# Kernel optimization log

Hardware: AMD Instinct MI355X
Metric: run time of the kernel (lower is better)

## Reference

```python
import jax, jax.numpy as jnp
import numpy as np
import math

C, NH, HD, L, P, FFN = 256, 8, 32, 1, 4, 512
H_BEV, W_BEV = 200, 100
NQ, BS, NV = 1000, 4, H_BEV * W_BEV
EPS = 1e-5


def _ln(x, g, b):
    m = x.mean(-1, keepdims=True)
    v = ((x - m) ** 2).mean(-1, keepdims=True)
    return (x - m) / jnp.sqrt(v + EPS) * g + b


def _mha(x, qpos, in_w, in_b, ow, ob):
    # nn.MultiheadAttention self-attention; key_pos = query_pos (shapes match)
    q = x + qpos
    k = x + qpos
    v = x
    wq, wk, wv = jnp.split(in_w, 3, axis=0)
    bq, bk, bv = jnp.split(in_b, 3, axis=0)
    bs, nq, _ = x.shape
    qh = (q @ wq.T + bq).reshape(bs, nq, NH, HD)
    kh = (k @ wk.T + bk).reshape(bs, nq, NH, HD)
    vh = (v @ wv.T + bv).reshape(bs, nq, NH, HD)
    scores = jnp.einsum('bqhd,bkhd->bhqk', qh, kh) / jnp.sqrt(jnp.float32(HD))
    attn = jax.nn.softmax(scores, axis=-1)
    out = jnp.einsum('bhqk,bkhd->bqhd', attn, vh).reshape(bs, nq, C)
    return out @ ow.T + ob


def _msdeform(x, qpos, value, ref, spatial_shapes, so_w, so_b, aw_w, aw_b, vp_w, vp_b, op_w, op_b):
    # Multi-scale deformable attention (single level), bilinear sampling with
    # align_corners=False convention and zero padding, as in the CUDA kernel.
    bs, nq, _ = x.shape
    q = x + qpos
    v = (value @ vp_w.T + vp_b).reshape(bs, NV, NH, HD).transpose(0, 2, 1, 3)  # [bs,nh,nv,hd]
    off = (q @ so_w.T + so_b).reshape(bs, nq, NH, L, P, 2)
    aw = jax.nn.softmax((q @ aw_w.T + aw_b).reshape(bs, nq, NH, L * P), axis=-1)
    aw = aw.reshape(bs, nq, NH, L, P)
    norm = jnp.stack([spatial_shapes[:, 1], spatial_shapes[:, 0]], -1).astype(jnp.float32)  # [L,2] = (W,H)
    loc = ref[:, :, None, :, None, :] + off / norm[None, None, None, :, None, :]  # [bs,nq,nh,L,P,2]
    loc = loc[:, :, :, 0]  # single level -> [bs,nq,nh,P,2]
    awp = aw[:, :, :, 0]   # [bs,nq,nh,P]
    x_im = loc[..., 0] * W_BEV - 0.5
    y_im = loc[..., 1] * H_BEV - 0.5
    x0 = jnp.floor(x_im)
    y0 = jnp.floor(y_im)
    lx = x_im - x0
    ly = y_im - y0
    x0i = x0.astype(jnp.int32)
    y0i = y0.astype(jnp.int32)
    acc = jnp.zeros((bs, NH, nq, P, HD), jnp.float32)
    for dy in (0, 1):
        for dx in (0, 1):
            xi = x0i + dx
            yi = y0i + dy
            w = (lx if dx else 1.0 - lx) * (ly if dy else 1.0 - ly)  # [bs,nq,nh,P]
            ok = ((xi >= 0) & (xi < W_BEV) & (yi >= 0) & (yi < H_BEV)).astype(jnp.float32)
            idx = jnp.clip(yi, 0, H_BEV - 1) * W_BEV + jnp.clip(xi, 0, W_BEV - 1)
            idx_t = idx.transpose(0, 2, 1, 3).reshape(bs, NH, nq * P)
            g = jnp.take_along_axis(v, idx_t[..., None], axis=2).reshape(bs, NH, nq, P, HD)
            acc = acc + g * (w * ok).transpose(0, 2, 1, 3)[..., None]
    out = (acc * awp.transpose(0, 2, 1, 3)[..., None]).sum(3)  # [bs,nh,nq,hd]
    out = out.transpose(0, 2, 1, 3).reshape(bs, nq, C)
    return out @ op_w.T + op_b


def setup_inputs() -> dict:
    key = jax.random.key(0)
    ks = jax.random.split(key, 24)
    f32 = jnp.float32

    def w(k, shp):
        fan = shp[-1]
        return (jax.random.normal(k, shp, f32) * (1.0 / np.sqrt(fan))).astype(f32)

    # sampling_offsets bias per _reset_parameters (radial grid init)
    thetas = np.arange(NH, dtype=np.float32) * (2.0 * math.pi / NH)
    grid = np.stack([np.cos(thetas), np.sin(thetas)], -1)
    grid = grid / np.abs(grid).max(-1, keepdims=True)
    grid = np.tile(grid[:, None, None, :], (1, L, P, 1))
    for i in range(P):
        grid[:, :, i, :] *= i + 1
    so_b = jnp.asarray(grid.reshape(-1), f32)

    return {
        'query': jax.random.normal(ks[0], (NQ, BS, C), f32),
        'value': jax.random.normal(ks[1], (NV, BS, C), f32),
        'query_pos': jax.random.normal(ks[2], (NQ, BS, C), f32),
        'reference_points': jax.random.uniform(ks[3], (BS, NQ, L, 2), f32),
        'spatial_shapes': jnp.array([[H_BEV, W_BEV]], jnp.int32),
        'level_start_index': jnp.zeros((L,), jnp.int32),
        'in_proj_w': w(ks[4], (3 * C, C)),
        'in_proj_b': jnp.zeros((3 * C,), f32),
        'mha_ow': w(ks[5], (C, C)),
        'mha_ob': jnp.zeros((C,), f32),
        'so_w': w(ks[6], (NH * L * P * 2, C)) * 0.01,
        'so_b': so_b,
        'aw_w': w(ks[7], (NH * L * P, C)) * 0.01,
        'aw_b': jnp.zeros((NH * L * P,), f32),
        'vp_w': w(ks[8], (C, C)),
        'vp_b': jnp.zeros((C,), f32),
        'op_w': w(ks[9], (C, C)),
        'op_b': jnp.zeros((C,), f32),
        'ffn_w1': w(ks[10], (FFN, C)),
        'ffn_b1': jnp.zeros((FFN,), f32),
        'ffn_w2': w(ks[11], (C, FFN)),
        'ffn_b2': jnp.zeros((C,), f32),
        'ln1_g': jnp.ones((C,), f32), 'ln1_b': jnp.zeros((C,), f32),
        'ln2_g': jnp.ones((C,), f32), 'ln2_b': jnp.zeros((C,), f32),
        'ln3_g': jnp.ones((C,), f32), 'ln3_b': jnp.zeros((C,), f32),
    }


def reference(query, value, query_pos, reference_points, spatial_shapes, level_start_index,
              in_proj_w, in_proj_b, mha_ow, mha_ob, so_w, so_b, aw_w, aw_b,
              vp_w, vp_b, op_w, op_b, ffn_w1, ffn_b1, ffn_w2, ffn_b2,
              ln1_g, ln1_b, ln2_g, ln2_b, ln3_g, ln3_b):
    # batch_first=False: (seq, bs, C) -> (bs, seq, C)
    x = query.transpose(1, 0, 2)
    val = value.transpose(1, 0, 2)
    qpos = query_pos.transpose(1, 0, 2)
    # self_attn -> norm (residual inside attn wrapper; dropout=0 in eval)
    x = _ln(x + _mha(x, qpos, in_proj_w, in_proj_b, mha_ow, mha_ob), ln1_g, ln1_b)
    # cross_attn (MSDeformAttn) -> norm
    x = _ln(x + _msdeform(x, qpos, val, reference_points, spatial_shapes,
                          so_w, so_b, aw_w, aw_b, vp_w, vp_b, op_w, op_b), ln2_g, ln2_b)
    # ffn -> norm
    h = jax.nn.relu(x @ ffn_w1.T + ffn_b1) @ ffn_w2.T + ffn_b2
    x = _ln(x + h, ln3_g, ln3_b)
    return x.transpose(1, 0, 2)
```

## Files before the change

### kernel.cpp

```cpp
#include <hip/hip_runtime.h>
#include <hip/hip_bf16.h>
#include <cmath>

#define BS   4
#define NQ   1000
#define CDIM 256
#define NH   8
#define HD   32
#define NVAL 20000
#define FFND 512
#define PN   4
#define WBEV 100
#define HBEV 200
#define TK   32

typedef __bf16 v8bf __attribute__((ext_vector_type(8)));
typedef float  v4f  __attribute__((ext_vector_type(4)));

__device__ __forceinline__ void gload_lds16(const void* g, void* l) {
    __builtin_amdgcn_global_load_lds(
        (const __attribute__((address_space(1))) unsigned int*)g,
        (__attribute__((address_space(3))) unsigned int*)l, 16, 0, 0);
}

__device__ __forceinline__ void vgemm_block(
    int vb, const float* __restrict__ value, const __bf16* __restrict__ Wv,
    const float* __restrict__ bv, __bf16* __restrict__ vpj, char* smem)
{
    __bf16* As = (__bf16*)smem;
    __bf16* Bs = (__bf16*)(smem + 16384);
    int tid = threadIdx.x;
    int wave = tid >> 6, lane = tid & 63, quad = lane >> 4, n16 = lane & 15;
    int bm = (vb >> 1) * 128, bn = (vb & 1) * 128;
    int wm = (wave & 1) * 64, wn = (wave >> 1) * 64;
    v4f acc[4][4] = {};

    for (int k0 = 0; k0 < 256; k0 += 64) {
        float4 fa[4][2];
        #pragma unroll
        for (int i = 0; i < 4; i++) {
            int e = i * 256 + tid;
            int r = e >> 3, c = (e & 7) ^ (r & 7);
            const float* p = value + (long)(bm + r) * 256 + k0 + c * 8;
            fa[i][0] = *(const float4*)p;
            fa[i][1] = *(const float4*)(p + 4);
        }
        __syncthreads();
        #pragma unroll
        for (int i = 0; i < 4; i++) {
            int e = i * 256 + tid;
            v8bf v;
            v[0] = (__bf16)fa[i][0].x; v[1] = (__bf16)fa[i][0].y;
            v[2] = (__bf16)fa[i][0].z; v[3] = (__bf16)fa[i][0].w;
            v[4] = (__bf16)fa[i][1].x; v[5] = (__bf16)fa[i][1].y;
            v[6] = (__bf16)fa[i][1].z; v[7] = (__bf16)fa[i][1].w;
            *(v8bf*)(As + e * 8) = v;
        }
        #pragma unroll
        for (int i = 0; i < 4; i++) {
            int e = i * 256 + tid;
            int r = e >> 3, c = (e & 7) ^ (r & 7);
            gload_lds16(Wv + (long)(bn + r) * 256 + k0 + c * 8, Bs + e * 8);
        }
        __syncthreads();
        #pragma unroll
        for (int s = 0; s < 2; s++) {
            v8bf af[4], bfr[4];
            #pragma unroll
            for (int mi = 0; mi < 4; mi++) {
                int row = wm + mi * 16 + n16;
                af[mi] = *(v8bf*)&As[row * 64 + (((quad + s * 4) ^ (row & 7))) * 8];
            }
            #pragma unroll
            for (int nj = 0; nj < 4; nj++) {
                int row = wn + nj * 16 + n16;
                bfr[nj] = *(v8bf*)&Bs[row * 64 + (((quad + s * 4) ^ (row & 7))) * 8];
            }
            #pragma unroll
            for (int mi = 0; mi < 4; mi++)
                #pragma unroll
                for (int nj = 0; nj < 4; nj++)
                    acc[mi][nj] = __builtin_amdgcn_mfma_f32_16x16x32_bf16(af[mi], bfr[nj], acc[mi][nj], 0, 0, 0);
        }
    }
    #pragma unroll
    for (int mi = 0; mi < 4; mi++) {
        #pragma unroll
        for (int r = 0; r < 4; r++) {
            int m = bm + wm + mi * 16 + quad * 4 + r;
            #pragma unroll
            for (int nj = 0; nj < 4; nj++) {
                int nn = bn + wn + nj * 16 + n16;
                vpj[(long)m * 256 + nn] = (__bf16)(acc[mi][nj][r] + bv[nn]);
            }
        }
    }
}

__global__ __launch_bounds__(256) void prep_all_kernel(
    const float* __restrict__ query, const float* __restrict__ qpos,
    const float* __restrict__ in_w, const float* __restrict__ mha_ow,
    const float* __restrict__ vp_w, const float* __restrict__ op_w,
    const float* __restrict__ ffn_w1, const float* __restrict__ ffn_w2,
    const float* __restrict__ so_w, const float* __restrict__ aw_w,
    const float* __restrict__ so_b, const float* __restrict__ aw_b,
    float* __restrict__ x, float* __restrict__ qpos_t,
    __bf16* __restrict__ x_bf, __bf16* __restrict__ xq_bf,
    __bf16* __restrict__ wb, __bf16* __restrict__ wsmall,
    float* __restrict__ bsmall)
{
    int blk = blockIdx.x, tid = threadIdx.x;
    if (blk < 640) {
        long e = ((long)blk * 256 + tid) * 4;
        const float* src; long off;
        if      (e < 196608) { src = in_w;   off = e; }
        else if (e < 262144) { src = mha_ow; off = e - 196608; }
        else if (e < 327680) { src = vp_w;   off = e - 262144; }
        else if (e < 393216) { src = op_w;   off = e - 327680; }
        else if (e < 524288) { src = ffn_w1; off = e - 393216; }
        else                 { src = ffn_w2; off = e - 524288; }
        float4 v = *(const float4*)(src + off);
        __bf16* d = wb + e;
        d[0] = (__bf16)v.x; d[1] = (__bf16)v.y; d[2] = (__bf16)v.z; d[3] = (__bf16)v.w;
    } else if (blk < 4640) {
        int qb = blk - 640;
        int q = qb / BS, b = qb % BS;
        float qv = query[(q * BS + b) * CDIM + tid];
        float pv = qpos [(q * BS + b) * CDIM + tid];
        int o = (b * NQ + q) * CDIM + tid;
        x[o] = qv; qpos_t[o] = pv;
        x_bf[o] = (__bf16)qv; xq_bf[o] = (__bf16)(qv + pv);
    } else if (blk < 4672) {
        long e = ((long)(blk - 4640) * 256 + tid) * 4;
        int row = (int)(e >> 8), col = (int)(e & 255);
        float4 v = {0.f, 0.f, 0.f, 0.f};
        if (row < 64)      v = *(const float4*)(so_w + row * 256 + col);
        else if (row < 96) v = *(const float4*)(aw_w + (row - 64) * 256 + col);
        __bf16* d = wsmall + e;
        d[0] = (__bf16)v.x; d[1] = (__bf16)v.y; d[2] = (__bf16)v.z; d[3] = (__bf16)v.w;
    } else {
        if (tid < 128) bsmall[tid] = tid < 64 ? so_b[tid] : (tid < 96 ? aw_b[tid - 64] : 0.f);
    }
}

template<int TBM, int TBN, bool RIDE>
__global__ __launch_bounds__(256) void mgemm_kernel(
    const __bf16* __restrict__ A, const __bf16* __restrict__ W,
    const float* __restrict__ bias, float* __restrict__ Yf,
    __bf16* __restrict__ Yb, int M, int N, int K, int relu, int nx, int nprim,
    const float* __restrict__ value, const __bf16* __restrict__ Wv,
    const float* __restrict__ bv, __bf16* __restrict__ vpj, int voff)
{
    constexpr int PRIM = TBM * 64 * 2 + TBN * 64 * 2;
    constexpr int SZ = RIDE ? (PRIM > 32768 ? PRIM : 32768) : PRIM;
    __shared__ __align__(16) char smem[SZ];
    if (RIDE && (int)blockIdx.x >= nprim) {
        vgemm_block(blockIdx.x - nprim + voff, value, Wv, bv, vpj, smem);
        return;
    }
    constexpr int WMF = TBM / 32;
    constexpr int WNF = TBN / 32;
    __bf16* As = (__bf16*)smem;
    __bf16* Bs = (__bf16*)(smem + TBM * 128);
    int bm = (blockIdx.x / nx) * TBM, bn = (blockIdx.x % nx) * TBN;
    int tid = threadIdx.x;
    int wave = tid >> 6, lane = tid & 63, quad = lane >> 4, n16 = lane & 15;
    int wm = (wave & 1) * (TBM / 2), wn = (wave >> 1) * (TBN / 2);
    v4f acc[WMF][WNF] = {};

    for (int k0 = 0; k0 < K; k0 += 64) {
        __syncthreads();
        #pragma unroll
        for (int i = 0; i < TBM * 8 / 256; i++) {
            int e = i * 256 + tid;
            int r = e >> 3, c = (e & 7) ^ (r & 7);
            int row = bm + r; if (row > M - 1) row = M - 1;
            gload_lds16(A + (long)row * K + k0 + c * 8, As + e * 8);
        }
        #pragma unroll
        for (int i = 0; i < TBN * 8 / 256; i++) {
            int e = i * 256 + tid;
            int r = e >> 3, c = (e & 7) ^ (r & 7);
            gload_lds16(W + (long)(bn + r) * K + k0 + c * 8, Bs + e * 8);
        }
        __syncthreads();
        #pragma unroll
        for (int s = 0; s < 2; s++) {
            v8bf af[WMF], bfr[WNF];
            #pragma unroll
            for (int mi = 0; mi < WMF; mi++) {
                int row = wm + mi * 16 + n16;
                af[mi] = *(v8bf*)&As[row * 64 + (((quad + s * 4) ^ (row & 7))) * 8];
            }
            #pragma unroll
            for (int nj = 0; nj < WNF; nj++) {
                int row = wn + nj * 16 + n16;
                bfr[nj] = *(v8bf*)&Bs[row * 64 + (((quad + s * 4) ^ (row & 7))) * 8];
            }
            #pragma unroll
            for (int mi = 0; mi < WMF; mi++)
                #pragma unroll
                for (int nj = 0; nj < WNF; nj++)
                    acc[mi][nj] = __builtin_amdgcn_mfma_f32_16x16x32_bf16(af[mi], bfr[nj], acc[mi][nj], 0, 0, 0);
        }
    }

    #pragma unroll
    for (int mi = 0; mi < WMF; mi++) {
        #pragma unroll
        for (int r = 0; r < 4; r++) {
            int m = bm + wm + mi * 16 + quad * 4 + r;
            if (m >= M) continue;
            #pragma unroll
            for (int nj = 0; nj < WNF; nj++) {
                int nn = bn + wn + nj * 16 + n16;
                if (nn >= N) continue;
                float v = acc[mi][nj][r] + bias[nn];
                if (relu) v = fmaxf(v, 0.f);
                if (Yf) Yf[(long)m * N + nn] = v;
                if (Yb) Yb[(long)m * N + nn] = (__bf16)v;
            }
        }
    }
}

__global__ __launch_bounds__(256) void qkvv_kernel(
    const __bf16* __restrict__ xq, const __bf16* __restrict__ xv,
    const __bf16* __restrict__ W, const float* __restrict__ bias,
    __bf16* __restrict__ qk, __bf16* __restrict__ vh,
    const float* __restrict__ value, const __bf16* __restrict__ Wv,
    const float* __restrict__ bv, __bf16* __restrict__ vpj, int voff)
{
    __shared__ __align__(16) char smem[32768];
    int tid = threadIdx.x;
    if (blockIdx.x >= 756) {
        vgemm_block(blockIdx.x - 756 + voff, value, Wv, bv, vpj, smem);
        return;
    }
    int blk = blockIdx.x;
    int bn = (blk % 12) * 64, bm = (blk / 12) * 64;
    __bf16* As = (__bf16*)smem;
    __bf16* Bs = (__bf16*)(smem + 8192);
    const __bf16* A = (bn < 512) ? xq : xv;
    int wave = tid >> 6, lane = tid & 63, quad = lane >> 4, n16 = lane & 15;
    int wm = (wave & 1) * 32, wn = (wave >> 1) * 32;
    v4f acc[2][2] = {};

    for (int k0 = 0; k0 < 256; k0 += 64) {
        __syncthreads();
        #pragma unroll
        for (int i = 0; i < 2; i++) {
            int e = i * 256 + tid;
            int r = e >> 3, c = (e & 7) ^ (r & 7);
            int row = bm + r; if (row > BS * NQ - 1) row = BS * NQ - 1;
            gload_lds16(A + (long)row * 256 + k0 + c * 8, As + e * 8);
        }
        #pragma unroll
        for (int i = 0; i < 2; i++) {
            int e = i * 256 + tid;
            int r = e >> 3, c = (e & 7) ^ (r & 7);
            gload_lds16(W + (long)(bn + r) * 256 + k0 + c * 8, Bs + e * 8);
        }
        __syncthreads();
        #pragma unroll
        for (int s = 0; s < 2; s++) {
            v8bf af[2], bfr[2];
            #pragma unroll
            for (int mi = 0; mi < 2; mi++) {
                int row = wm + mi * 16 + n16;
                af[mi] = *(v8bf*)&As[row * 64 + (((quad + s * 4) ^ (row & 7))) * 8];
            }
            #pragma unroll
            for (int nj = 0; nj < 2; nj++) {
                int row = wn + nj * 16 + n16;
                bfr[nj] = *(v8bf*)&Bs[row * 64 + (((quad + s * 4) ^ (row & 7))) * 8];
            }
            #pragma unroll
            for (int mi = 0; mi < 2; mi++)
                #pragma unroll
                for (int nj = 0; nj < 2; nj++)
                    acc[mi][nj] = __builtin_amdgcn_mfma_f32_16x16x32_bf16(af[mi], bfr[nj], acc[mi][nj], 0, 0, 0);
        }
    }

    #pragma unroll
    for (int mi = 0; mi < 2; mi++) {
        #pragma unroll
        for (int r = 0; r < 4; r++) {
            int m = bm + wm + mi * 16 + quad * 4 + r;
            if (m >= BS * NQ) continue;
            #pragma unroll
            for (int nj = 0; nj < 2; nj++) {
                int nn = bn + wn + nj * 16 + n16;
                float v = acc[mi][nj][r] + bias[nn];
                if (nn < 512) qk[(long)m * 512 + nn] = (__bf16)v;
                else          vh[(long)m * 256 + (nn - 512)] = (__bf16)v;
            }
        }
    }
}

__global__ __launch_bounds__(256) void fattnv_kernel(
    const __bf16* __restrict__ qk, const __bf16* __restrict__ vh,
    __bf16* __restrict__ aout,
    const float* __restrict__ value, const __bf16* __restrict__ Wv,
    const float* __restrict__ bv, __bf16* __restrict__ vpj, int voff)
{
    __shared__ __align__(16) char smem[32768];
    int tid = threadIdx.x;
    if (blockIdx.x >= 512) {
        vgemm_block(blockIdx.x - 512 + voff, value, Wv, bv, vpj, smem);
        return;
    }
    int fb = blockIdx.x;
    int qt = fb & 15, h = (fb >> 4) & 7, b = fb >> 7;
    __bf16* Ks = (__bf16*)smem;
    __bf16* Vt = (__bf16*)(smem + 5120);
    __bf16* Pl = (__bf16*)(smem + 10240);
    int wave = tid >> 6, lane = tid & 63, quad = lane >> 4, n = lane & 15;
    int q0 = qt * 64 + wave * 16;
    const float scale = 0.17677669529663687f;
    const float M0 = 8.0f;

    int qrow = q0 + n; if (qrow > NQ - 1) qrow = NQ - 1;
    v8bf aq = *(const v8bf*)(qk + (long)(b * NQ + qrow) * 512 + h * HD + quad * 8);

    v4f o0 = {}, o1 = {};
    float lp[4] = {0.f, 0.f, 0.f, 0.f};

    int sv = tid >> 7;
    int t2 = tid & 127;
    int key = t2 >> 2;
    int d8 = (t2 & 3) * 8;
    int vcol = key ^ (((d8 >> 3) & 1) << 4);

    auto loadtile = [&](int k0) -> v8bf {
        int krow = k0 + key; if (krow > NQ - 1) krow = NQ - 1;
        const __bf16* p = sv ? (vh + (long)(b * NQ + krow) * CDIM + h * HD + d8)
                             : (qk + (long)(b * NQ + krow) * 512 + 256 + h * HD + d8);
        return *(const v8bf*)p;
    };

    v8bf stg = loadtile(0);
    int pb = 0;
    for (int k0 = 0; k0 < NQ; k0 += TK) {
        if (sv == 0) {
            *(v8bf*)&Ks[(pb * TK + key) * 40 + d8] = stg;
        } else {
            #pragma unroll
            for (int j = 0; j < 8; j++) Vt[(pb * HD + d8 + j) * 40 + vcol] = stg[j];
        }
        if (k0 + TK < NQ) stg = loadtile(k0 + TK);
        __syncthreads();

        v8bf bk0 = *(v8bf*)&Ks[(pb * TK + n) * 40 + quad * 8];
        v8bf bk1 = *(v8bf*)&Ks[(pb * TK + 16 + n) * 40 + quad * 8];
        v4f z = {};
        v4f S0 = __builtin_amdgcn_mfma_f32_16x16x32_bf16(aq, bk0, z, 0, 0, 0);
        v4f S1 = __builtin_amdgcn_mfma_f32_16x16x32_bf16(aq, bk1, z, 0, 0, 0);

        bool last = (k0 + TK > NQ);
        float p0[4], p1[4];
        #pragma unroll
        for (int r = 0; r < 4; r++) {
            p0[r] = __expf(fmaf(S0[r], scale, -M0));
            p1[r] = __expf(fmaf(S1[r], scale, -M0));
            if (last) {
                if (k0 + n >= NQ)      p0[r] = 0.f;
                if (k0 + 16 + n >= NQ) p1[r] = 0.f;
            }
            lp[r] += p0[r] + p1[r];
        }
        #pragma unroll
        for (int r = 0; r < 4; r++) {
            Pl[(wave * 16 + quad * 4 + r) * 40 + n]      = (__bf16)p0[r];
            Pl[(wave * 16 + quad * 4 + r) * 40 + 16 + n] = (__bf16)p1[r];
        }
        asm volatile("s_waitcnt lgkmcnt(0)" ::: "memory");
        v8bf ap = *(v8bf*)&Pl[(wave * 16 + n) * 40 + quad * 8];
        int vc = (quad * 8) ^ (((n >> 3) & 1) << 4);
        v8bf bv0 = *(v8bf*)&Vt[(pb * HD + n) * 40 + vc];
        v8bf bv1 = *(v8bf*)&Vt[(pb * HD + 16 + n) * 40 + vc];
        o0 = __builtin_amdgcn_mfma_f32_16x16x32_bf16(ap, bv0, o0, 0, 0, 0);
        o1 = __builtin_amdgcn_mfma_f32_16x16x32_bf16(ap, bv1, o1, 0, 0, 0);
        pb ^= 1;
    }

    #pragma unroll
    for (int r = 0; r < 4; r++) {
        float l = lp[r];
        #pragma unroll
        for (int off = 1; off < 16; off <<= 1) l += __shfl_xor(l, off, 16);
        int q = q0 + quad * 4 + r;
        if (q < NQ) {
            float invl = 1.0f / l;
            __bf16* op = aout + ((long)(b * NQ + q) * CDIM + h * HD);
            op[n]      = (__bf16)(o0[r] * invl);
            op[16 + n] = (__bf16)(o1[r] * invl);
        }
    }
}

template<int KD, int MODE, bool RIDE>
__global__ __launch_bounds__(256) void gemmln_kernel(
    const __bf16* __restrict__ A, const __bf16* __restrict__ W,
    const float* __restrict__ bias, const float* __restrict__ res,
    const float* __restrict__ g, const float* __restrict__ beta,
    const float* __restrict__ qpos_t,
    float* __restrict__ outf, __bf16* __restrict__ outb,
    const float* __restrict__ value, const __bf16* __restrict__ Wv,
    const float* __restrict__ bv, __bf16* __restrict__ vpj, int voff)
{
    __shared__ __align__(16) char smem[35328];
    int tid = threadIdx.x;
    if (RIDE && blockIdx.x >= 250) {
        vgemm_block(blockIdx.x - 250 + voff, value, Wv, bv, vpj, smem);
        return;
    }
    __bf16* As = (__bf16*)smem;
    __bf16* Bs = (__bf16*)(smem + 2048);
    float* redS = (float*)(smem + 34816);
    float* redQ = redS + 64;
    int bm = blockIdx.x * 16;
    int wave = tid >> 6, lane = tid & 63, quad = lane >> 4, n16 = lane & 15;
    int wn = wave * 64;
    v4f acc[4] = {};

    for (int k0 = 0; k0 < KD; k0 += 64) {
        __syncthreads();
        if (tid < 128) {
            int e = tid;
            int r = e >> 3, c = (e & 7) ^ (r & 7);
            gload_lds16(A + (long)(bm + r) * KD + k0 + c * 8, As + e * 8);
        }
        #pragma unroll
        for (int i = 0; i < 8; i++) {
            int e = i * 256 + tid;
            int r = e >> 3, c = (e & 7) ^ (r & 7);
            gload_lds16(W + (long)r * KD + k0 + c * 8, Bs + e * 8);
        }
        __syncthreads();
        #pragma unroll
        for (int s = 0; s < 2; s++) {
            v8bf af = *(v8bf*)&As[n16 * 64 + (((quad + s * 4) ^ (n16 & 7))) * 8];
            #pragma unroll
            for (int nj = 0; nj < 4; nj++) {
                int row = wn + nj * 16 + n16;
                v8bf bfr = *(v8bf*)&Bs[row * 64 + (((quad + s * 4) ^ (row & 7))) * 8];
                acc[nj] = __builtin_amdgcn_mfma_f32_16x16x32_bf16(af, bfr, acc[nj], 0, 0, 0);
            }
        }
    }

    float y[4][4], s1[4] = {}, s2[4] = {};
    #pragma unroll
    for (int r = 0; r < 4; r++) {
        int m = bm + quad * 4 + r;
        #pragma unroll
        for (int nj = 0; nj < 4; nj++) {
            int nn = wn + nj * 16 + n16;
            float v = acc[nj][r] + bias[nn] + res[(long)m * 256 + nn];
            y[r][nj] = v;
            s1[r] += v; s2[r] += v * v;
        }
    }
    #pragma unroll
    for (int r = 0; r < 4; r++) {
        #pragma unroll
        for (int off = 1; off < 16; off <<= 1) {
            s1[r] += __shfl_xor(s1[r], off, 16);
            s2[r] += __shfl_xor(s2[r], off, 16);
        }
    }
    if (n16 == 0) {
        #pragma unroll
        for (int r = 0; r < 4; r++) {
            redS[wave * 16 + quad * 4 + r] = s1[r];
            redQ[wave * 16 + quad * 4 + r] = s2[r];
        }
    }
    __syncthreads();
    #pragma unroll
    for (int r = 0; r < 4; r++) {
        int mr = quad * 4 + r;
        float ts = redS[mr] + redS[16 + mr] + redS[32 + mr] + redS[48 + mr];
        float tq = redQ[mr] + redQ[16 + mr] + redQ[32 + mr] + redQ[48 + mr];
        float mean = ts * (1.0f / 256.0f);
        float var = tq * (1.0f / 256.0f) - mean * mean;
        float rinv = rsqrtf(var + 1e-5f);
        int m = bm + mr;
        #pragma unroll
        for (int nj = 0; nj < 4; nj++) {
            int nn = wn + nj * 16 + n16;
            float o = (y[r][nj] - mean) * rinv * g[nn] + beta[nn];
            if (MODE == 0) {
                outf[(long)m * 256 + nn] = o;
                outb[(long)m * 256 + nn] = (__bf16)(o + qpos_t[(long)m * 256 + nn]);
            } else if (MODE == 1) {
                outf[(long)m * 256 + nn] = o;
                outb[(long)m * 256 + nn] = (__bf16)o;
            } else {
                int b = m / NQ, q = m % NQ;
                outf[(long)(q * BS + b) * 256 + nn] = o;
            }
        }
    }
}

__global__ __launch_bounds__(256) void msds_kernel(
    const __bf16* __restrict__ vproj, const float* __restrict__ soaw,
    const float* __restrict__ refp, __bf16* __restrict__ out)
{
    int bq = blockIdx.x; int b = bq / NQ; int q = bq % NQ;
    int t = threadIdx.x; int h = t / HD; int d = t % HD;
    float rx = refp[(b * NQ + q) * 2 + 0];
    float ry = refp[(b * NQ + q) * 2 + 1];
    const float* rowp = soaw + (long)(b * NQ + q) * 96;
    const float* offp = rowp + h * 8;
    const float* awp  = rowp + 64 + h * 4;
    float a0 = awp[0], a1 = awp[1], a2 = awp[2], a3 = awp[3];
    float m = fmaxf(fmaxf(a0, a1), fmaxf(a2, a3));
    float e0 = __expf(a0 - m), e1 = __expf(a1 - m), e2 = __expf(a2 - m), e3 = __expf(a3 - m);
    float invs = 1.0f / (e0 + e1 + e2 + e3);
    float acc = 0.f;
    #pragma unroll
    for (int p = 0; p < PN; p++) {
        float ew = (p == 0 ? e0 : p == 1 ? e1 : p == 2 ? e2 : e3) * invs;
        float xim = rx * (float)WBEV + offp[p * 2 + 0] - 0.5f;
        float yim = ry * (float)HBEV + offp[p * 2 + 1] - 0.5f;
        float x0f = floorf(xim), y0f = floorf(yim);
        float lx = xim - x0f, ly = yim - y0f;
        int x0 = (int)x0f, y0 = (int)y0f;
        float gsum = 0.f;
        #pragma unroll
        for (int dy = 0; dy < 2; dy++) {
            #pragma unroll
            for (int dx = 0; dx < 2; dx++) {
                int xi = x0 + dx, yi = y0 + dy;
                float w = (dx ? lx : 1.f - lx) * (dy ? ly : 1.f - ly);
                bool ok = (xi >= 0 && xi < WBEV && yi >= 0 && yi < HBEV);
                int xc = min(max(xi, 0), WBEV - 1);
                int yc = min(max(yi, 0), HBEV - 1);
                int idx = yc * WBEV + xc;
                float gv = (float)vproj[((long)(idx * BS + b)) * CDIM + h * HD + d];
                gsum += (ok ? w : 0.f) * gv;
            }
        }
        acc += ew * gsum;
    }
    out[(b * NQ + q) * CDIM + h * HD + d] = (__bf16)acc;
}

extern "C" void kernel_launch(void* const* d_in, const int* in_sizes, int n_in,
                              void* d_out, int out_size, void* d_ws, size_t ws_size,
                              hipStream_t stream) {
    const float* query = (const float*)d_in[0];
    const float* value = (const float*)d_in[1];
    const float* qpos  = (const float*)d_in[2];
    const float* refp  = (const float*)d_in[3];
    const float* in_w  = (const float*)d_in[6];
    const float* in_b  = (const float*)d_in[7];
    const float* mha_ow = (const float*)d_in[8];
    const float* mha_ob = (const float*)d_in[9];
    const float* so_w  = (const float*)d_in[10];
    const float* so_b  = (const float*)d_in[11];
    const float* aw_w  = (const float*)d_in[12];
    const float* aw_b  = (const float*)d_in[13];
    const float* vp_w  = (const float*)d_in[14];
    const float* vp_b  = (const float*)d_in[15];
    const float* op_w  = (const float*)d_in[16];
    const float* op_b  = (const float*)d_in[17];
    const float* ffn_w1 = (const float*)d_in[18];
    const float* ffn_b1 = (const float*)d_in[19];
    const float* ffn_w2 = (const float*)d_in[20];
    const float* ffn_b2 = (const float*)d_in[21];
    const float* ln1_g = (const float*)d_in[22];
    const float* ln1_b = (const float*)d_in[23];
    const float* ln2_g = (const float*)d_in[24];
    const float* ln2_b = (const float*)d_in[25];
    const float* ln3_g = (const float*)d_in[26];
    const float* ln3_b = (const float*)d_in[27];
    float* out = (float*)d_out;

    const long NTOK = (long)BS * NQ * CDIM;

    float* x      = (float*)d_ws;
    float* qpos_t = x + NTOK;
    float* x1     = qpos_t + NTOK;
    float* x2     = x1 + NTOK;
    float* soaw   = x2 + NTOK;
    float* bsmall = soaw + (long)BS * NQ * 96;
    __bf16* x_bf   = (__bf16*)(bsmall + 128);
    __bf16* xq_bf  = x_bf + NTOK;
    __bf16* qk_bf  = xq_bf + NTOK;
    __bf16* vh_bf  = qk_bf + 2 * NTOK;
    __bf16* aA_bf  = vh_bf + NTOK;
    __bf16* x2_bf  = aA_bf + NTOK;
    __bf16* h1_bf  = x2_bf + NTOK;
    __bf16* vpj_bf = h1_bf + 2 * NTOK;
    __bf16* wb     = vpj_bf + (long)BS * NVAL * CDIM;
    __bf16* inw_b  = wb;
    __bf16* mow_b  = wb + 196608;
    __bf16* vpw_b  = wb + 262144;
    __bf16* opw_b  = wb + 327680;
    __bf16* fw1_b  = wb + 393216;
    __bf16* fw2_b  = wb + 524288;
    __bf16* wsmall = wb + 655360;

    dim3 blk(256);

    prep_all_kernel<<<4673, blk, 0, stream>>>(
        query, qpos, in_w, mha_ow, vp_w, op_w, ffn_w1, ffn_w2,
        so_w, aw_w, so_b, aw_b,
        x, qpos_t, x_bf, xq_bf, wb, wsmall, bsmall);

    qkvv_kernel<<<1069, blk, 0, stream>>>(xq_bf, x_bf, inw_b, in_b, qk_bf, vh_bf,
                                          value, vpw_b, vp_b, vpj_bf, 0);

    fattnv_kernel<<<825, blk, 0, stream>>>(qk_bf, vh_bf, aA_bf,
                                           value, vpw_b, vp_b, vpj_bf, 313);

    gemmln_kernel<256, 0, true><<<563, blk, 0, stream>>>(
        aA_bf, mow_b, mha_ob, x, ln1_g, ln1_b, qpos_t, x1, xq_bf,
        value, vpw_b, vp_b, vpj_bf, 626);

    mgemm_kernel<32, 128, true><<<436, blk, 0, stream>>>(
        xq_bf, wsmall, bsmall, soaw, nullptr, BS * NQ, 96, 256, 0, 1, 125,
        value, vpw_b, vp_b, vpj_bf, 939);

    msds_kernel<<<BS * NQ, blk, 0, stream>>>(vpj_bf, soaw, refp, aA_bf);

    gemmln_kernel<256, 1, false><<<250, blk, 0, stream>>>(
        aA_bf, opw_b, op_b, x1, ln2_g, ln2_b, nullptr, x2, x2_bf,
        nullptr, nullptr, nullptr, nullptr, 0);

    mgemm_kernel<64, 64, false><<<504, blk, 0, stream>>>(
        x2_bf, fw1_b, ffn_b1, nullptr, h1_bf, BS * NQ, 512, 256, 1, 8, 504,
        nullptr, nullptr, nullptr, nullptr, 0);

    gemmln_kernel<512, 2, false><<<250, blk, 0, stream>>>(
        h1_bf, fw2_b, ffn_b2, x2, ln3_g, ln3_b, nullptr, out, nullptr,
        nullptr, nullptr, nullptr, nullptr, 0);
}
```

Measured before the change: 279.0 us.

## Fuse LN1 with sampling-offset GEMM and deformable sampling with output projection

Several stages are restructured into fewer launches. The LN1 GEMM now also computes the sampling-offset and attention-weight projection from an LDS-resident x+qpos tile. Deformable sampling is fused with the output projection and LN2 in one kernel. The value-projection side blocks are retiled to 64x256, and the flash-attention key tile grows from 32 to 64. These changes remove two launches and intermediate round trips, at the cost of more LDS per block and changed occupancy and load balance for the blocks that carry the value projection.

```diff
diff --git a/kernel.cpp b/kernel.cpp
--- a/kernel.cpp
+++ b/kernel.cpp
@@ -12,7 +12,7 @@
 #define PN   4
 #define WBEV 100
 #define HBEV 200
-#define TK   32
+#define TK   64
 
 typedef __bf16 v8bf __attribute__((ext_vector_type(8)));
 typedef float  v4f  __attribute__((ext_vector_type(4)));
@@ -23,22 +23,22 @@
         (__attribute__((address_space(3))) unsigned int*)l, 16, 0, 0);
 }
 
-__device__ __forceinline__ void vgemm_block(
+__device__ __forceinline__ void vgemm64_block(
     int vb, const float* __restrict__ value, const __bf16* __restrict__ Wv,
     const float* __restrict__ bv, __bf16* __restrict__ vpj, char* smem)
 {
     __bf16* As = (__bf16*)smem;
-    __bf16* Bs = (__bf16*)(smem + 16384);
+    __bf16* Bs = (__bf16*)(smem + 8192);
     int tid = threadIdx.x;
     int wave = tid >> 6, lane = tid & 63, quad = lane >> 4, n16 = lane & 15;
-    int bm = (vb >> 1) * 128, bn = (vb & 1) * 128;
-    int wm = (wave & 1) * 64, wn = (wave >> 1) * 64;
-    v4f acc[4][4] = {};
+    int bm = vb * 64;
+    int wm = (wave & 1) * 32, wn = (wave >> 1) * 128;
+    v4f acc[2][8] = {};
 
     for (int k0 = 0; k0 < 256; k0 += 64) {
-        float4 fa[4][2];
-        #pragma unroll
-        for (int i = 0; i < 4; i++) {
+        float4 fa[2][2];
+        #pragma unroll
+        for (int i = 0; i < 2; i++) {
             int e = i * 256 + tid;
             int r = e >> 3, c = (e & 7) ^ (r & 7);
             const float* p = value + (long)(bm + r) * 256 + k0 + c * 8;
@@ -47,7 +47,7 @@
         }
         __syncthreads();
         #pragma unroll
-        for (int i = 0; i < 4; i++) {
+        for (int i = 0; i < 2; i++) {
             int e = i * 256 + tid;
             v8bf v;
             v[0] = (__bf16)fa[i][0].x; v[1] = (__bf16)fa[i][0].y;
@@ -57,40 +57,40 @@
             *(v8bf*)(As + e * 8) = v;
         }
         #pragma unroll
-        for (int i = 0; i < 4; i++) {
-            int e = i * 256 + tid;
-            int r = e >> 3, c = (e & 7) ^ (r & 7);
-            gload_lds16(Wv + (long)(bn + r) * 256 + k0 + c * 8, Bs + e * 8);
+        for (int i = 0; i < 8; i++) {
+            int e = i * 256 + tid;
+            int r = e >> 3, c = (e & 7) ^ (r & 7);
+            gload_lds16(Wv + (long)r * 256 + k0 + c * 8, Bs + e * 8);
         }
         __syncthreads();
         #pragma unroll
         for (int s = 0; s < 2; s++) {
-            v8bf af[4], bfr[4];
-            #pragma unroll
-            for (int mi = 0; mi < 4; mi++) {
+            v8bf af[2], bfr[8];
+            #pragma unroll
+            for (int mi = 0; mi < 2; mi++) {
                 int row = wm + mi * 16 + n16;
                 af[mi] = *(v8bf*)&As[row * 64 + (((quad + s * 4) ^ (row & 7))) * 8];
             }
             #pragma unroll
-            for (int nj = 0; nj < 4; nj++) {
+            for (int nj = 0; nj < 8; nj++) {
                 int row = wn + nj * 16 + n16;
                 bfr[nj] = *(v8bf*)&Bs[row * 64 + (((quad + s * 4) ^ (row & 7))) * 8];
             }
             #pragma unroll
-            for (int mi = 0; mi < 4; mi++)
+            for (int mi = 0; mi < 2; mi++)
                 #pragma unroll
-                for (int nj = 0; nj < 4; nj++)
+                for (int nj = 0; nj < 8; nj++)
                     acc[mi][nj] = __builtin_amdgcn_mfma_f32_16x16x32_bf16(af[mi], bfr[nj], acc[mi][nj], 0, 0, 0);
         }
     }
     #pragma unroll
-    for (int mi = 0; mi < 4; mi++) {
+    for (int mi = 0; mi < 2; mi++) {
         #pragma unroll
         for (int r = 0; r < 4; r++) {
             int m = bm + wm + mi * 16 + quad * 4 + r;
             #pragma unroll
-            for (int nj = 0; nj < 4; nj++) {
-                int nn = bn + wn + nj * 16 + n16;
+            for (int nj = 0; nj < 8; nj++) {
+                int nn = wn + nj * 16 + n16;
                 vpj[(long)m * 256 + nn] = (__bf16)(acc[mi][nj][r] + bv[nn]);
             }
         }
@@ -143,21 +143,467 @@
     }
 }
 
-template<int TBM, int TBN, bool RIDE>
-__global__ __launch_bounds__(256) void mgemm_kernel(
-    const __bf16* __restrict__ A, const __bf16* __restrict__ W,
-    const float* __restrict__ bias, float* __restrict__ Yf,
-    __bf16* __restrict__ Yb, int M, int N, int K, int relu, int nx, int nprim,
+__global__ __launch_bounds__(256) void qkvv_kernel(
+    const __bf16* __restrict__ xq, const __bf16* __restrict__ xv,
+    const __bf16* __restrict__ W, const float* __restrict__ bias,
+    __bf16* __restrict__ qk, __bf16* __restrict__ vh,
     const float* __restrict__ value, const __bf16* __restrict__ Wv,
     const float* __restrict__ bv, __bf16* __restrict__ vpj, int voff)
 {
-    constexpr int PRIM = TBM * 64 * 2 + TBN * 64 * 2;
-    constexpr int SZ = RIDE ? (PRIM > 32768 ? PRIM : 32768) : PRIM;
+    __shared__ __align__(16) char smem[40960];
+    int tid = threadIdx.x;
+    if ((int)blockIdx.x >= 756) {
+        vgemm64_block(blockIdx.x - 756 + voff, value, Wv, bv, vpj, smem);
+        return;
+    }
+    int blk = blockIdx.x;
+    int bn = (blk % 12) * 64, bm = (blk / 12) * 64;
+    __bf16* As = (__bf16*)smem;
+    __bf16* Bs = (__bf16*)(smem + 8192);
+    const __bf16* A = (bn < 512) ? xq : xv;
+    int wave = tid >> 6, lane = tid & 63, quad = lane >> 4, n16 = lane & 15;
+    int wm = (wave & 1) * 32, wn = (wave >> 1) * 32;
+    v4f acc[2][2] = {};
+
+    for (int k0 = 0; k0 < 256; k0 += 64) {
+        __syncthreads();
+        #pragma unroll
+        for (int i = 0; i < 2; i++) {
+            int e = i * 256 + tid;
+            int r = e >> 3, c = (e & 7) ^ (r & 7);
+            int row = bm + r; if (row > BS * NQ - 1) row = BS * NQ - 1;
+            gload_lds16(A + (long)row * 256 + k0 + c * 8, As + e * 8);
+        }
+        #pragma unroll
+        for (int i = 0; i < 2; i++) {
+            int e = i * 256 + tid;
+            int r = e >> 3, c = (e & 7) ^ (r & 7);
+            gload_lds16(W + (long)(bn + r) * 256 + k0 + c * 8, Bs + e * 8);
+        }
+        __syncthreads();
+        #pragma unroll
+        for (int s = 0; s < 2; s++) {
+            v8bf af[2], bfr[2];
+            #pragma unroll
+            for (int mi = 0; mi < 2; mi++) {
+                int row = wm + mi * 16 + n16;
+                af[mi] = *(v8bf*)&As[row * 64 + (((quad + s * 4) ^ (row & 7))) * 8];
+            }
+            #pragma unroll
+            for (int nj = 0; nj < 2; nj++) {
+                int row = wn + nj * 16 + n16;
+                bfr[nj] = *(v8bf*)&Bs[row * 64 + (((quad + s * 4) ^ (row & 7))) * 8];
+            }
+            #pragma unroll
+            for (int mi = 0; mi < 2; mi++)
+                #pragma unroll
+                for (int nj = 0; nj < 2; nj++)
+                    acc[mi][nj] = __builtin_amdgcn_mfma_f32_16x16x32_bf16(af[mi], bfr[nj], acc[mi][nj], 0, 0, 0);
+        }
+    }
+
+    #pragma unroll
+    for (int mi = 0; mi < 2; mi++) {
+        #pragma unroll
+        for (int r = 0; r < 4; r++) {
+            int m = bm + wm + mi * 16 + quad * 4 + r;
+            if (m >= BS * NQ) continue;
+            #pragma unroll
+            for (int nj = 0; nj < 2; nj++) {
+                int nn = bn + wn + nj * 16 + n16;
+                float v = acc[mi][nj][r] + bias[nn];
+                if (nn < 512) qk[(long)m * 512 + nn] = (__bf16)v;
+                else          vh[(long)m * 256 + (nn - 512)] = (__bf16)v;
+            }
+        }
+    }
+}
+
+__global__ __launch_bounds__(256) void fattnv_kernel(
+    const __bf16* __restrict__ qk, const __bf16* __restrict__ vh,
+    __bf16* __restrict__ aout,
+    const float* __restrict__ value, const __bf16* __restrict__ Wv,
+    const float* __restrict__ bv, __bf16* __restrict__ vpj, int voff)
+{
+    __shared__ __align__(16) char smem[40960];
+    int tid = threadIdx.x;
+    if ((int)blockIdx.x >= 512) {
+        vgemm64_block(blockIdx.x - 512 + voff, value, Wv, bv, vpj, smem);
+        return;
+    }
+    int fb = blockIdx.x;
+    int qt = fb & 15, h = (fb >> 4) & 7, b = fb >> 7;
+    __bf16* Ks = (__bf16*)smem;
+    __bf16* Vt = (__bf16*)(smem + 10240);
+    __bf16* Pl = (__bf16*)(smem + 19456);
+    int wave = tid >> 6, lane = tid & 63, quad = lane >> 4, n = lane & 15;
+    int q0 = qt * 64 + wave * 16;
+    const float scale = 0.17677669529663687f;
+    const float M0 = 8.0f;
+
+    int qrow = q0 + n; if (qrow > NQ - 1) qrow = NQ - 1;
+    v8bf aq = *(const v8bf*)(qk + (long)(b * NQ + qrow) * 512 + h * HD + quad * 8);
+
+    v4f o0 = {}, o1 = {};
+    float lp[4] = {0.f, 0.f, 0.f, 0.f};
+
+    int sv = tid >> 7;
+    int t2 = tid & 127;
+    int key = t2 & 63;
+    int d16 = (t2 >> 6) * 16;
+
+    v8bf stg0, stg1;
+    auto loadtile = [&](int k0) {
+        int krow = k0 + key; if (krow > NQ - 1) krow = NQ - 1;
+        const __bf16* p = sv ? (vh + (long)(b * NQ + krow) * CDIM + h * HD + d16)
+                             : (qk + (long)(b * NQ + krow) * 512 + 256 + h * HD + d16);
+        stg0 = *(const v8bf*)p;
+        stg1 = *(const v8bf*)(p + 8);
+    };
+
+    loadtile(0);
+    int pb = 0;
+    for (int k0 = 0; k0 < NQ; k0 += TK) {
+        if (sv == 0) {
+            *(v8bf*)&Ks[(pb * 64 + key) * 40 + d16]     = stg0;
+            *(v8bf*)&Ks[(pb * 64 + key) * 40 + d16 + 8] = stg1;
+        } else {
+            #pragma unroll
+            for (int j = 0; j < 8; j++) {
+                Vt[(pb * 32 + d16 + j) * 72 + key]            = stg0[j];
+                Vt[(pb * 32 + d16 + 8 + j) * 72 + (key ^ 16)] = stg1[j];
+            }
+        }
+        if (k0 + TK < NQ) loadtile(k0 + TK);
+        __syncthreads();
+
+        v8bf bk0 = *(v8bf*)&Ks[(pb * 64 +      n) * 40 + quad * 8];
+        v8bf bk1 = *(v8bf*)&Ks[(pb * 64 + 16 + n) * 40 + quad * 8];
+        v8bf bk2 = *(v8bf*)&Ks[(pb * 64 + 32 + n) * 40 + quad * 8];
+        v8bf bk3 = *(v8bf*)&Ks[(pb * 64 + 48 + n) * 40 + quad * 8];
+        v4f z = {};
+        v4f S0 = __builtin_amdgcn_mfma_f32_16x16x32_bf16(aq, bk0, z, 0, 0, 0);
+        v4f S1 = __builtin_amdgcn_mfma_f32_16x16x32_bf16(aq, bk1, z, 0, 0, 0);
+        v4f S2 = __builtin_amdgcn_mfma_f32_16x16x32_bf16(aq, bk2, z, 0, 0, 0);
+        v4f S3 = __builtin_amdgcn_mfma_f32_16x16x32_bf16(aq, bk3, z, 0, 0, 0);
+
+        bool last = (k0 + TK > NQ);
+        float p0[4], p1[4], p2[4], p3[4];
+        #pragma unroll
+        for (int r = 0; r < 4; r++) {
+            p0[r] = __expf(fmaf(S0[r], scale, -M0));
+            p1[r] = __expf(fmaf(S1[r], scale, -M0));
+            p2[r] = __expf(fmaf(S2[r], scale, -M0));
+            p3[r] = __expf(fmaf(S3[r], scale, -M0));
+            if (last) {
+                if (k0 + 32 + n >= NQ) p2[r] = 0.f;
+                if (k0 + 48 + n >= NQ) p3[r] = 0.f;
+            }
+            lp[r] += p0[r] + p1[r] + p2[r] + p3[r];
+        }
+        #pragma unroll
+        for (int r = 0; r < 4; r++) {
+            __bf16* pp = &Pl[(wave * 16 + quad * 4 + r) * 72];
+            pp[n]      = (__bf16)p0[r];
+            pp[16 + n] = (__bf16)p1[r];
+            pp[32 + n] = (__bf16)p2[r];
+            pp[48 + n] = (__bf16)p3[r];
+        }
+        asm volatile("s_waitcnt lgkmcnt(0)" ::: "memory");
+        v8bf ap0 = *(v8bf*)&Pl[(wave * 16 + n) * 72 + quad * 8];
+        v8bf ap1 = *(v8bf*)&Pl[(wave * 16 + n) * 72 + 32 + quad * 8];
+        int swz = ((n >> 3) & 1) << 4;
+        int c0 = (quad * 8) ^ swz;
+        int c1 = (32 + quad * 8) ^ swz;
+        v8bf bv00 = *(v8bf*)&Vt[(pb * 32 +      n) * 72 + c0];
+        v8bf bv01 = *(v8bf*)&Vt[(pb * 32 +      n) * 72 + c1];
+        v8bf bv10 = *(v8bf*)&Vt[(pb * 32 + 16 + n) * 72 + c0];
+        v8bf bv11 = *(v8bf*)&Vt[(pb * 32 + 16 + n) * 72 + c1];
+        o0 = __builtin_amdgcn_mfma_f32_16x16x32_bf16(ap0, bv00, o0, 0, 0, 0);
+        o0 = __builtin_amdgcn_mfma_f32_16x16x32_bf16(ap1, bv01, o0, 0, 0, 0);
+        o1 = __builtin_amdgcn_mfma_f32_16x16x32_bf16(ap0, bv10, o1, 0, 0, 0);
+        o1 = __builtin_amdgcn_mfma_f32_16x16x32_bf16(ap1, bv11, o1, 0, 0, 0);
+        pb ^= 1;
+    }
+
+    #pragma unroll
+    for (int r = 0; r < 4; r++) {
+        float l = lp[r];
+        #pragma unroll
+        for (int off = 1; off < 16; off <<= 1) l += __shfl_xor(l, off, 16);
+        int q = q0 + quad * 4 + r;
+        if (q < NQ) {
+            float invl = 1.0f / l;
+            __bf16* op = aout + ((long)(b * NQ + q) * CDIM + h * HD);
+            op[n]      = (__bf16)(o0[r] * invl);
+            op[16 + n] = (__bf16)(o1[r] * invl);
+        }
+    }
+}
+
+__global__ __launch_bounds__(256) void gln1s_kernel(
+    const __bf16* __restrict__ A, const __bf16* __restrict__ W,
+    const float* __restrict__ bias, const float* __restrict__ res,
+    const float* __restrict__ g, const float* __restrict__ beta,
+    const float* __restrict__ qpos_t,
+    const __bf16* __restrict__ Wsm, const float* __restrict__ bsm,
+    float* __restrict__ outf, float* __restrict__ soawO,
+    const float* __restrict__ value, const __bf16* __restrict__ Wv,
+    const float* __restrict__ bv, __bf16* __restrict__ vpj, int voff)
+{
+    __shared__ __align__(16) char smem[43776];
+    int tid = threadIdx.x;
+    if ((int)blockIdx.x >= 250) {
+        vgemm64_block(blockIdx.x - 250 + voff, value, Wv, bv, vpj, smem);
+        return;
+    }
+    __bf16* As  = (__bf16*)smem;
+    __bf16* Bs  = (__bf16*)(smem + 2048);
+    __bf16* Axq = (__bf16*)(smem + 34816);
+    float* redS = (float*)(smem + 43264);
+    float* redQ = redS + 64;
+    int bm = blockIdx.x * 16;
+    int wave = tid >> 6, lane = tid & 63, quad = lane >> 4, n16 = lane & 15;
+    int wn = wave * 64;
+    v4f acc[4] = {};
+
+    for (int k0 = 0; k0 < 256; k0 += 64) {
+        __syncthreads();
+        if (tid < 128) {
+            int e = tid;
+            int r = e >> 3, c = (e & 7) ^ (r & 7);
+            gload_lds16(A + (long)(bm + r) * 256 + k0 + c * 8, As + e * 8);
+        }
+        #pragma unroll
+        for (int i = 0; i < 8; i++) {
+            int e = i * 256 + tid;
+            int r = e >> 3, c = (e & 7) ^ (r & 7);
+            gload_lds16(W + (long)r * 256 + k0 + c * 8, Bs + e * 8);
+        }
+        __syncthreads();
+        #pragma unroll
+        for (int s = 0; s < 2; s++) {
+            v8bf af = *(v8bf*)&As[n16 * 64 + (((quad + s * 4) ^ (n16 & 7))) * 8];
+            #pragma unroll
+            for (int nj = 0; nj < 4; nj++) {
+                int row = wn + nj * 16 + n16;
+                v8bf bfr = *(v8bf*)&Bs[row * 64 + (((quad + s * 4) ^ (row & 7))) * 8];
+                acc[nj] = __builtin_amdgcn_mfma_f32_16x16x32_bf16(af, bfr, acc[nj], 0, 0, 0);
+            }
+        }
+    }
+
+    float y[4][4], s1[4] = {}, s2[4] = {};
+    #pragma unroll
+    for (int r = 0; r < 4; r++) {
+        int m = bm + quad * 4 + r;
+        #pragma unroll
+        for (int nj = 0; nj < 4; nj++) {
+            int nn = wn + nj * 16 + n16;
+            float v = acc[nj][r] + bias[nn] + res[(long)m * 256 + nn];
+            y[r][nj] = v;
+            s1[r] += v; s2[r] += v * v;
+        }
+    }
+    #pragma unroll
+    for (int r = 0; r < 4; r++) {
+        #pragma unroll
+        for (int off = 1; off < 16; off <<= 1) {
+            s1[r] += __shfl_xor(s1[r], off, 16);
+            s2[r] += __shfl_xor(s2[r], off, 16);
+        }
+    }
+    if (n16 == 0) {
+        #pragma unroll
+        for (int r = 0; r < 4; r++) {
+            redS[wave * 16 + quad * 4 + r] = s1[r];
+            redQ[wave * 16 + quad * 4 + r] = s2[r];
+        }
+    }
+    __syncthreads();
+    #pragma unroll
+    for (int r = 0; r < 4; r++) {
+        int mr = quad * 4 + r;
+        float ts = redS[mr] + redS[16 + mr] + redS[32 + mr] + redS[48 + mr];
+        float tq = redQ[mr] + redQ[16 + mr] + redQ[32 + mr] + redQ[48 + mr];
+        float mean = ts * (1.0f / 256.0f);
+        float var = tq * (1.0f / 256.0f) - mean * mean;
+        float rinv = rsqrtf(var + 1e-5f);
+        int m = bm + mr;
+        #pragma unroll
+        for (int nj = 0; nj < 4; nj++) {
+            int nn = wn + nj * 16 + n16;
+            float o = (y[r][nj] - mean) * rinv * g[nn] + beta[nn];
+            outf[(long)m * 256 + nn] = o;
+            Axq[mr * 264 + nn] = (__bf16)(o + qpos_t[(long)m * 256 + nn]);
+        }
+    }
+    __syncthreads();
+    if (wave < 3) {
+        v4f sacc[2] = {};
+        #pragma unroll
+        for (int k0 = 0; k0 < 256; k0 += 32) {
+            v8bf af = *(v8bf*)&Axq[n16 * 264 + k0 + quad * 8];
+            #pragma unroll
+            for (int t = 0; t < 2; t++) {
+                int col = wave * 32 + t * 16 + n16;
+                v8bf bw = *(const v8bf*)(Wsm + (long)col * 256 + k0 + quad * 8);
+                sacc[t] = __builtin_amdgcn_mfma_f32_16x16x32_bf16(af, bw, sacc[t], 0, 0, 0);
+            }
+        }
+        #pragma unroll
+        for (int t = 0; t < 2; t++)
+            #pragma unroll
+            for (int r = 0; r < 4; r++) {
+                int mm = bm + quad * 4 + r;
+                int col = wave * 32 + t * 16 + n16;
+                soawO[(long)mm * 96 + col] = sacc[t][r] + bsm[col];
+            }
+    }
+}
+
+__global__ __launch_bounds__(256) void msdsop_kernel(
+    const __bf16* __restrict__ vproj, const float* __restrict__ soaw,
+    const float* __restrict__ refp,
+    const __bf16* __restrict__ W, const float* __restrict__ bias,
+    const float* __restrict__ res, const float* __restrict__ g,
+    const float* __restrict__ beta,
+    float* __restrict__ outf, __bf16* __restrict__ outb)
+{
+    __shared__ __align__(16) char smem[41472];
+    __bf16* As4 = (__bf16*)smem;
+    __bf16* Bs  = (__bf16*)(smem + 8192);
+    float* redS = (float*)(smem + 40960);
+    float* redQ = redS + 64;
+    int tid = threadIdx.x;
+    int bm = blockIdx.x * 16;
+    int h = tid >> 5, d = tid & 31;
+
+    #pragma unroll 4
+    for (int r = 0; r < 16; r++) {
+        int m = bm + r;
+        int bb = m / NQ;
+        float rx = refp[m * 2 + 0];
+        float ry = refp[m * 2 + 1];
+        const float* rowp = soaw + (long)m * 96;
+        const float* offp = rowp + h * 8;
+        const float* awp  = rowp + 64 + h * 4;
+        float a0 = awp[0], a1 = awp[1], a2 = awp[2], a3 = awp[3];
+        float mx = fmaxf(fmaxf(a0, a1), fmaxf(a2, a3));
+        float e0 = __expf(a0 - mx), e1 = __expf(a1 - mx);
+        float e2 = __expf(a2 - mx), e3 = __expf(a3 - mx);
+        float invs = 1.0f / (e0 + e1 + e2 + e3);
+        float acc = 0.f;
+        #pragma unroll
+        for (int p = 0; p < PN; p++) {
+            float ew = (p == 0 ? e0 : p == 1 ? e1 : p == 2 ? e2 : e3) * invs;
+            float xim = rx * (float)WBEV + offp[p * 2 + 0] - 0.5f;
+            float yim = ry * (float)HBEV + offp[p * 2 + 1] - 0.5f;
+            float x0f = floorf(xim), y0f = floorf(yim);
+            float lx = xim - x0f, ly = yim - y0f;
+            int x0 = (int)x0f, y0 = (int)y0f;
+            float gsum = 0.f;
+            #pragma unroll
+            for (int dy = 0; dy < 2; dy++) {
+                #pragma unroll
+                for (int dx = 0; dx < 2; dx++) {
+                    int xi = x0 + dx, yi = y0 + dy;
+                    float w = (dx ? lx : 1.f - lx) * (dy ? ly : 1.f - ly);
+                    bool ok = (xi >= 0 && xi < WBEV && yi >= 0 && yi < HBEV);
+                    int xc = min(max(xi, 0), WBEV - 1);
+                    int yc = min(max(yi, 0), HBEV - 1);
+                    int idx = yc * WBEV + xc;
+                    float gv = (float)vproj[((long)(idx * BS + bb)) * CDIM + h * HD + d];
+                    gsum += (ok ? w : 0.f) * gv;
+                }
+            }
+            acc += ew * gsum;
+        }
+        int cg = (tid >> 3) & 7, jj = tid & 7, kc = tid >> 6;
+        As4[kc * 1024 + r * 64 + ((cg ^ (r & 7)) << 3) + jj] = (__bf16)acc;
+    }
+    __syncthreads();
+
+    int wave = tid >> 6, lane = tid & 63, quad = lane >> 4, n16 = lane & 15;
+    int wn = wave * 64;
+    v4f acc2[4] = {};
+    for (int k0 = 0; k0 < 256; k0 += 64) {
+        __syncthreads();
+        #pragma unroll
+        for (int i = 0; i < 8; i++) {
+            int e = i * 256 + tid;
+            int r = e >> 3, c = (e & 7) ^ (r & 7);
+            gload_lds16(W + (long)r * 256 + k0 + c * 8, Bs + e * 8);
+        }
+        __syncthreads();
+        int kc = k0 >> 6;
+        #pragma unroll
+        for (int s = 0; s < 2; s++) {
+            v8bf af = *(v8bf*)&As4[kc * 1024 + n16 * 64 + (((quad + s * 4) ^ (n16 & 7))) * 8];
+            #pragma unroll
+            for (int nj = 0; nj < 4; nj++) {
+                int row = wn + nj * 16 + n16;
+                v8bf bfr = *(v8bf*)&Bs[row * 64 + (((quad + s * 4) ^ (row & 7))) * 8];
+                acc2[nj] = __builtin_amdgcn_mfma_f32_16x16x32_bf16(af, bfr, acc2[nj], 0, 0, 0);
+            }
+        }
+    }
+
+    float y[4][4], s1[4] = {}, s2[4] = {};
+    #pragma unroll
+    for (int r = 0; r < 4; r++) {
+        int m = bm + quad * 4 + r;
+        #pragma unroll
+        for (int nj = 0; nj < 4; nj++) {
+            int nn = wn + nj * 16 + n16;
+            float v = acc2[nj][r] + bias[nn] + res[(long)m * 256 + nn];
+            y[r][nj] = v;
+            s1[r] += v; s2[r] += v * v;
+        }
+    }
+    #pragma unroll
+    for (int r = 0; r < 4; r++) {
+        #pragma unroll
+        for (int off = 1; off < 16; off <<= 1) {
+            s1[r] += __shfl_xor(s1[r], off, 16);
+            s2[r] += __shfl_xor(s2[r], off, 16);
+        }
+    }
+    if (n16 == 0) {
+        #pragma unroll
+        for (int r = 0; r < 4; r++) {
+            redS[wave * 16 + quad * 4 + r] = s1[r];
+            redQ[wave * 16 + quad * 4 + r] = s2[r];
+        }
+    }
+    __syncthreads();
+    #pragma unroll
+    for (int r = 0; r < 4; r++) {
+        int mr = quad * 4 + r;
+        float ts = redS[mr] + redS[16 + mr] + redS[32 + mr] + redS[48 + mr];
+        float tq = redQ[mr] + redQ[16 + mr] + redQ[32 + mr] + redQ[48 + mr];
+        float mean = ts * (1.0f / 256.0f);
+        float var = tq * (1.0f / 256.0f) - mean * mean;
+        float rinv = rsqrtf(var + 1e-5f);
+        int m = bm + mr;
+        #pragma unroll
+        for (int nj = 0; nj < 4; nj++) {
+            int nn = wn + nj * 16 + n16;
+            float o = (y[r][nj] - mean) * rinv * g[nn] + beta[nn];
+            outf[(long)m * 256 + nn] = o;
+            outb[(long)m * 256 + nn] = (__bf16)o;
+        }
+    }
+}
+
+template<int TBM, int TBN>
+__global__ __launch_bounds__(256) void mgemm_kernel(
+    const __bf16* __restrict__ A, const __bf16* __restrict__ W,
+    const float* __restrict__ bias, __bf16* __restrict__ Yb,
+    int M, int N, int K, int relu, int nx)
+{
+    constexpr int SZ = TBM * 128 + TBN * 128;
     __shared__ __align__(16) char smem[SZ];
-    if (RIDE && (int)blockIdx.x >= nprim) {
-        vgemm_block(blockIdx.x - nprim + voff, value, Wv, bv, vpj, smem);
-        return;
-    }
     constexpr int WMF = TBM / 32;
     constexpr int WNF = TBN / 32;
     __bf16* As = (__bf16*)smem;
@@ -217,227 +663,41 @@
                 if (nn >= N) continue;
                 float v = acc[mi][nj][r] + bias[nn];
                 if (relu) v = fmaxf(v, 0.f);
-                if (Yf) Yf[(long)m * N + nn] = v;
-                if (Yb) Yb[(long)m * N + nn] = (__bf16)v;
-            }
-        }
-    }
-}
-
-__global__ __launch_bounds__(256) void qkvv_kernel(
-    const __bf16* __restrict__ xq, const __bf16* __restrict__ xv,
-    const __bf16* __restrict__ W, const float* __restrict__ bias,
-    __bf16* __restrict__ qk, __bf16* __restrict__ vh,
-    const float* __restrict__ value, const __bf16* __restrict__ Wv,
-    const float* __restrict__ bv, __bf16* __restrict__ vpj, int voff)
-{
-    __shared__ __align__(16) char smem[32768];
-    int tid = threadIdx.x;
-    if (blockIdx.x >= 756) {
-        vgemm_block(blockIdx.x - 756 + voff, value, Wv, bv, vpj, smem);
-        return;
-    }
-    int blk = blockIdx.x;
-    int bn = (blk % 12) * 64, bm = (blk / 12) * 64;
-    __bf16* As = (__bf16*)smem;
-    __bf16* Bs = (__bf16*)(smem + 8192);
-    const __bf16* A = (bn < 512) ? xq : xv;
-    int wave = tid >> 6, lane = tid & 63, quad = lane >> 4, n16 = lane & 15;
-    int wm = (wave & 1) * 32, wn = (wave >> 1) * 32;
-    v4f acc[2][2] = {};
-
-    for (int k0 = 0; k0 < 256; k0 += 64) {
-        __syncthreads();
-        #pragma unroll
-        for (int i = 0; i < 2; i++) {
-            int e = i * 256 + tid;
-            int r = e >> 3, c = (e & 7) ^ (r & 7);
-            int row = bm + r; if (row > BS * NQ - 1) row = BS * NQ - 1;
-            gload_lds16(A + (long)row * 256 + k0 + c * 8, As + e * 8);
-        }
-        #pragma unroll
-        for (int i = 0; i < 2; i++) {
-            int e = i * 256 + tid;
-            int r = e >> 3, c = (e & 7) ^ (r & 7);
-            gload_lds16(W + (long)(bn + r) * 256 + k0 + c * 8, Bs + e * 8);
-        }
-        __syncthreads();
-        #pragma unroll
-        for (int s = 0; s < 2; s++) {
-            v8bf af[2], bfr[2];
-            #pragma unroll
-            for (int mi = 0; mi < 2; mi++) {
-                int row = wm + mi * 16 + n16;
-                af[mi] = *(v8bf*)&As[row * 64 + (((quad + s * 4) ^ (row & 7))) * 8];
-            }
-            #pragma unroll
-            for (int nj = 0; nj < 2; nj++) {
-                int row = wn + nj * 16 + n16;
-                bfr[nj] = *(v8bf*)&Bs[row * 64 + (((quad + s * 4) ^ (row & 7))) * 8];
-            }
-            #pragma unroll
-            for (int mi = 0; mi < 2; mi++)
-                #pragma unroll
-                for (int nj = 0; nj < 2; nj++)
-                    acc[mi][nj] = __builtin_amdgcn_mfma_f32_16x16x32_bf16(af[mi], bfr[nj], acc[mi][nj], 0, 0, 0);
-        }
-    }
-
-    #pragma unroll
-    for (int mi = 0; mi < 2; mi++) {
-        #pragma unroll
-        for (int r = 0; r < 4; r++) {
-            int m = bm + wm + mi * 16 + quad * 4 + r;
-            if (m >= BS * NQ) continue;
-            #pragma unroll
-            for (int nj = 0; nj < 2; nj++) {
-                int nn = bn + wn + nj * 16 + n16;
-                float v = acc[mi][nj][r] + bias[nn];
-                if (nn < 512) qk[(long)m * 512 + nn] = (__bf16)v;
-                else          vh[(long)m * 256 + (nn - 512)] = (__bf16)v;
-            }
-        }
-    }
-}
-
-__global__ __launch_bounds__(256) void fattnv_kernel(
-    const __bf16* __restrict__ qk, const __bf16* __restrict__ vh,
-    __bf16* __restrict__ aout,
-    const float* __restrict__ value, const __bf16* __restrict__ Wv,
-    const float* __restrict__ bv, __bf16* __restrict__ vpj, int voff)
-{
-    __shared__ __align__(16) char smem[32768];
-    int tid = threadIdx.x;
-    if (blockIdx.x >= 512) {
-        vgemm_block(blockIdx.x - 512 + voff, value, Wv, bv, vpj, smem);
-        return;
-    }
-    int fb = blockIdx.x;
-    int qt = fb & 15, h = (fb >> 4) & 7, b = fb >> 7;
-    __bf16* Ks = (__bf16*)smem;
-    __bf16* Vt = (__bf16*)(smem + 5120);
-    __bf16* Pl = (__bf16*)(smem + 10240);
-    int wave = tid >> 6, lane = tid & 63, quad = lane >> 4, n = lane & 15;
-    int q0 = qt * 64 + wave * 16;
-    const float scale = 0.17677669529663687f;
-    const float M0 = 8.0f;
-
-    int qrow = q0 + n; if (qrow > NQ - 1) qrow = NQ - 1;
-    v8bf aq = *(const v8bf*)(qk + (long)(b * NQ + qrow) * 512 + h * HD + quad * 8);
-
-    v4f o0 = {}, o1 = {};
-    float lp[4] = {0.f, 0.f, 0.f, 0.f};
-
-    int sv = tid >> 7;
-    int t2 = tid & 127;
-    int key = t2 >> 2;
-    int d8 = (t2 & 3) * 8;
-    int vcol = key ^ (((d8 >> 3) & 1) << 4);
-
-    auto loadtile = [&](int k0) -> v8bf {
-        int krow = k0 + key; if (krow > NQ - 1) krow = NQ - 1;
-        const __bf16* p = sv ? (vh + (long)(b * NQ + krow) * CDIM + h * HD + d8)
-                             : (qk + (long)(b * NQ + krow) * 512 + 256 + h * HD + d8);
-        return *(const v8bf*)p;
-    };
-
-    v8bf stg = loadtile(0);
-    int pb = 0;
-    for (int k0 = 0; k0 < NQ; k0 += TK) {
-        if (sv == 0) {
-            *(v8bf*)&Ks[(pb * TK + key) * 40 + d8] = stg;
-        } else {
-            #pragma unroll
-            for (int j = 0; j < 8; j++) Vt[(pb * HD + d8 + j) * 40 + vcol] = stg[j];
-        }
-        if (k0 + TK < NQ) stg = loadtile(k0 + TK);
-        __syncthreads();
-
-        v8bf bk0 = *(v8bf*)&Ks[(pb * TK + n) * 40 + quad * 8];
-        v8bf bk1 = *(v8bf*)&Ks[(pb * TK + 16 + n) * 40 + quad * 8];
-        v4f z = {};
-        v4f S0 = __builtin_amdgcn_mfma_f32_16x16x32_bf16(aq, bk0, z, 0, 0, 0);
-        v4f S1 = __builtin_amdgcn_mfma_f32_16x16x32_bf16(aq, bk1, z, 0, 0, 0);
-
-        bool last = (k0 + TK > NQ);
-        float p0[4], p1[4];
-        #pragma unroll
-        for (int r = 0; r < 4; r++) {
-            p0[r] = __expf(fmaf(S0[r], scale, -M0));
-            p1[r] = __expf(fmaf(S1[r], scale, -M0));
-            if (last) {
-                if (k0 + n >= NQ)      p0[r] = 0.f;
-                if (k0 + 16 + n >= NQ) p1[r] = 0.f;
-            }
-            lp[r] += p0[r] + p1[r];
-        }
-        #pragma unroll
-        for (int r = 0; r < 4; r++) {
-            Pl[(wave * 16 + quad * 4 + r) * 40 + n]      = (__bf16)p0[r];
-            Pl[(wave * 16 + quad * 4 + r) * 40 + 16 + n] = (__bf16)p1[r];
-        }
-        asm volatile("s_waitcnt lgkmcnt(0)" ::: "memory");
-        v8bf ap = *(v8bf*)&Pl[(wave * 16 + n) * 40 + quad * 8];
-        int vc = (quad * 8) ^ (((n >> 3) & 1) << 4);
-        v8bf bv0 = *(v8bf*)&Vt[(pb * HD + n) * 40 + vc];
-        v8bf bv1 = *(v8bf*)&Vt[(pb * HD + 16 + n) * 40 + vc];
-        o0 = __builtin_amdgcn_mfma_f32_16x16x32_bf16(ap, bv0, o0, 0, 0, 0);
-        o1 = __builtin_amdgcn_mfma_f32_16x16x32_bf16(ap, bv1, o1, 0, 0, 0);
-        pb ^= 1;
-    }
-
-    #pragma unroll
-    for (int r = 0; r < 4; r++) {
-        float l = lp[r];
-        #pragma unroll
-        for (int off = 1; off < 16; off <<= 1) l += __shfl_xor(l, off, 16);
-        int q = q0 + quad * 4 + r;
-        if (q < NQ) {
-            float invl = 1.0f / l;
-            __bf16* op = aout + ((long)(b * NQ + q) * CDIM + h * HD);
-            op[n]      = (__bf16)(o0[r] * invl);
-            op[16 + n] = (__bf16)(o1[r] * invl);
-        }
-    }
-}
-
-template<int KD, int MODE, bool RIDE>
-__global__ __launch_bounds__(256) void gemmln_kernel(
+                Yb[(long)m * N + nn] = (__bf16)v;
+            }
+        }
+    }
+}
+
+__global__ __launch_bounds__(256) void gln3_kernel(
     const __bf16* __restrict__ A, const __bf16* __restrict__ W,
     const float* __restrict__ bias, const float* __restrict__ res,
     const float* __restrict__ g, const float* __restrict__ beta,
-    const float* __restrict__ qpos_t,
-    float* __restrict__ outf, __bf16* __restrict__ outb,
-    const float* __restrict__ value, const __bf16* __restrict__ Wv,
-    const float* __restrict__ bv, __bf16* __restrict__ vpj, int voff)
+    float* __restrict__ outf)
 {
     __shared__ __align__(16) char smem[35328];
-    int tid = threadIdx.x;
-    if (RIDE && blockIdx.x >= 250) {
-        vgemm_block(blockIdx.x - 250 + voff, value, Wv, bv, vpj, smem);
-        return;
-    }
     __bf16* As = (__bf16*)smem;
     __bf16* Bs = (__bf16*)(smem + 2048);
     float* redS = (float*)(smem + 34816);
     float* redQ = redS + 64;
+    int tid = threadIdx.x;
     int bm = blockIdx.x * 16;
     int wave = tid >> 6, lane = tid & 63, quad = lane >> 4, n16 = lane & 15;
     int wn = wave * 64;
     v4f acc[4] = {};
 
-    for (int k0 = 0; k0 < KD; k0 += 64) {
+    for (int k0 = 0; k0 < 512; k0 += 64) {
         __syncthreads();
         if (tid < 128) {
             int e = tid;
             int r = e >> 3, c = (e & 7) ^ (r & 7);
-            gload_lds16(A + (long)(bm + r) * KD + k0 + c * 8, As + e * 8);
+            gload_lds16(A + (long)(bm + r) * 512 + k0 + c * 8, As + e * 8);
         }
         #pragma unroll
         for (int i = 0; i < 8; i++) {
             int e = i * 256 + tid;
             int r = e >> 3, c = (e & 7) ^ (r & 7);
-            gload_lds16(W + (long)r * KD + k0 + c * 8, Bs + e * 8);
+            gload_lds16(W + (long)r * 512 + k0 + c * 8, Bs + e * 8);
         }
         __syncthreads();
         #pragma unroll
@@ -489,66 +749,14 @@
         float var = tq * (1.0f / 256.0f) - mean * mean;
         float rinv = rsqrtf(var + 1e-5f);
         int m = bm + mr;
+        int b = m / NQ, q = m - b * NQ;
         #pragma unroll
         for (int nj = 0; nj < 4; nj++) {
             int nn = wn + nj * 16 + n16;
             float o = (y[r][nj] - mean) * rinv * g[nn] + beta[nn];
-            if (MODE == 0) {
-                outf[(long)m * 256 + nn] = o;
-                outb[(long)m * 256 + nn] = (__bf16)(o + qpos_t[(long)m * 256 + nn]);
-            } else if (MODE == 1) {
-                outf[(long)m * 256 + nn] = o;
-                outb[(long)m * 256 + nn] = (__bf16)o;
-            } else {
-                int b = m / NQ, q = m % NQ;
-                outf[(long)(q * BS + b) * 256 + nn] = o;
-            }
-        }
-    }
-}
-
-__global__ __launch_bounds__(256) void msds_kernel(
-    const __bf16* __restrict__ vproj, const float* __restrict__ soaw,
-    const float* __restrict__ refp, __bf16* __restrict__ out)
-{
-    int bq = blockIdx.x; int b = bq / NQ; int q = bq % NQ;
-    int t = threadIdx.x; int h = t / HD; int d = t % HD;
-    float rx = refp[(b * NQ + q) * 2 + 0];
-    float ry = refp[(b * NQ + q) * 2 + 1];
-    const float* rowp = soaw + (long)(b * NQ + q) * 96;
-    const float* offp = rowp + h * 8;
-    const float* awp  = rowp + 64 + h * 4;
-    float a0 = awp[0], a1 = awp[1], a2 = awp[2], a3 = awp[3];
-    float m = fmaxf(fmaxf(a0, a1), fmaxf(a2, a3));
-    float e0 = __expf(a0 - m), e1 = __expf(a1 - m), e2 = __expf(a2 - m), e3 = __expf(a3 - m);
-    float invs = 1.0f / (e0 + e1 + e2 + e3);
-    float acc = 0.f;
-    #pragma unroll
-    for (int p = 0; p < PN; p++) {
-        float ew = (p == 0 ? e0 : p == 1 ? e1 : p == 2 ? e2 : e3) * invs;
-        float xim = rx * (float)WBEV + offp[p * 2 + 0] - 0.5f;
-        float yim = ry * (float)HBEV + offp[p * 2 + 1] - 0.5f;
-        float x0f = floorf(xim), y0f = floorf(yim);
-        float lx = xim - x0f, ly = yim - y0f;
-        int x0 = (int)x0f, y0 = (int)y0f;
-        float gsum = 0.f;
-        #pragma unroll
-        for (int dy = 0; dy < 2; dy++) {
-            #pragma unroll
-            for (int dx = 0; dx < 2; dx++) {
-                int xi = x0 + dx, yi = y0 + dy;
-                float w = (dx ? lx : 1.f - lx) * (dy ? ly : 1.f - ly);
-                bool ok = (xi >= 0 && xi < WBEV && yi >= 0 && yi < HBEV);
-                int xc = min(max(xi, 0), WBEV - 1);
-                int yc = min(max(yi, 0), HBEV - 1);
-                int idx = yc * WBEV + xc;
-                float gv = (float)vproj[((long)(idx * BS + b)) * CDIM + h * HD + d];
-                gsum += (ok ? w : 0.f) * gv;
-            }
-        }
-        acc += ew * gsum;
-    }
-    out[(b * NQ + q) * CDIM + h * HD + d] = (__bf16)acc;
+            outf[(long)(q * BS + b) * 256 + nn] = o;
+        }
+    }
 }
 
 extern "C" void kernel_launch(void* const* d_in, const int* in_sizes, int n_in,
@@ -614,31 +822,22 @@
         so_w, aw_w, so_b, aw_b,
         x, qpos_t, x_bf, xq_bf, wb, wsmall, bsmall);
 
-    qkvv_kernel<<<1069, blk, 0, stream>>>(xq_bf, x_bf, inw_b, in_b, qk_bf, vh_bf,
+    qkvv_kernel<<<1173, blk, 0, stream>>>(xq_bf, x_bf, inw_b, in_b, qk_bf, vh_bf,
                                           value, vpw_b, vp_b, vpj_bf, 0);
 
-    fattnv_kernel<<<825, blk, 0, stream>>>(qk_bf, vh_bf, aA_bf,
-                                           value, vpw_b, vp_b, vpj_bf, 313);
-
-    gemmln_kernel<256, 0, true><<<563, blk, 0, stream>>>(
-        aA_bf, mow_b, mha_ob, x, ln1_g, ln1_b, qpos_t, x1, xq_bf,
-        value, vpw_b, vp_b, vpj_bf, 626);
-
-    mgemm_kernel<32, 128, true><<<436, blk, 0, stream>>>(
-        xq_bf, wsmall, bsmall, soaw, nullptr, BS * NQ, 96, 256, 0, 1, 125,
-        value, vpw_b, vp_b, vpj_bf, 939);
-
-    msds_kernel<<<BS * NQ, blk, 0, stream>>>(vpj_bf, soaw, refp, aA_bf);
-
-    gemmln_kernel<256, 1, false><<<250, blk, 0, stream>>>(
-        aA_bf, opw_b, op_b, x1, ln2_g, ln2_b, nullptr, x2, x2_bf,
-        nullptr, nullptr, nullptr, nullptr, 0);
-
-    mgemm_kernel<64, 64, false><<<504, blk, 0, stream>>>(
-        x2_bf, fw1_b, ffn_b1, nullptr, h1_bf, BS * NQ, 512, 256, 1, 8, 504,
-        nullptr, nullptr, nullptr, nullptr, 0);
-
-    gemmln_kernel<512, 2, false><<<250, blk, 0, stream>>>(
-        h1_bf, fw2_b, ffn_b2, x2, ln3_g, ln3_b, nullptr, out, nullptr,
-        nullptr, nullptr, nullptr, nullptr, 0);
-}
+    fattnv_kernel<<<929, blk, 0, stream>>>(qk_bf, vh_bf, aA_bf,
+                                           value, vpw_b, vp_b, vpj_bf, 417);
+
+    gln1s_kernel<<<666, blk, 0, stream>>>(
+        aA_bf, mow_b, mha_ob, x, ln1_g, ln1_b, qpos_t, wsmall, bsmall,
+        x1, soaw, value, vpw_b, vp_b, vpj_bf, 834);
+
+    msdsop_kernel<<<250, blk, 0, stream>>>(
+        vpj_bf, soaw, refp, opw_b, op_b, x1, ln2_g, ln2_b, x2, x2_bf);
+
+    mgemm_kernel<64, 64><<<504, blk, 0, stream>>>(
+        x2_bf, fw1_b, ffn_b1, h1_bf, BS * NQ, 512, 256, 1, 8);
+
+    gln3_kernel<<<250, blk, 0, stream>>>(
+        h1_bf, fw2_b, ffn_b2, x2, ln3_g, ln3_b, out);
+}
```

Result: slower. 345.6 us (+23.9%).
